# Optimization experiments

Hardware: AMD Instinct MI355X
Metric: run time of the kernel (lower is better)

The kernel has to match this reference:

```python
import jax, jax.numpy as jnp
import numpy as np

N_NODES = 50000
N_EDGES = 800000
IN_F, HID_F, OUT_F = 96, 96, 32


def setup_inputs() -> dict:
    key = jax.random.key(0)
    k1, k2, k3, k4, k5 = jax.random.split(key, 5)
    x = jax.random.normal(k1, (N_NODES, IN_F), dtype=jnp.float32)
    src = jax.random.randint(k2, (N_EDGES,), 0, N_NODES, dtype=jnp.int32)
    dst = jax.random.randint(k3, (N_EDGES,), 0, N_NODES, dtype=jnp.int32)
    W1 = jax.random.normal(k4, (IN_F, HID_F), dtype=jnp.float32) / np.sqrt(IN_F)
    b1 = jnp.zeros((HID_F,), dtype=jnp.float32)
    W2 = jax.random.normal(k5, (HID_F, OUT_F), dtype=jnp.float32) / np.sqrt(HID_F)
    b2 = jnp.zeros((OUT_F,), dtype=jnp.float32)
    return {"x": x, "src": src, "dst": dst, "W1": W1, "b1": b1, "W2": W2, "b2": b2}


def _graph_conv(src, dst, n_nodes, h, W, b):
    # DGL GraphConv, norm='both': D_out^{-1/2} A D_in^{-1/2} h W + b
    ones = jnp.ones((src.shape[0],), dtype=h.dtype)
    deg_out = jax.ops.segment_sum(ones, src, num_segments=n_nodes)  # src out-degree
    deg_in = jax.ops.segment_sum(ones, dst, num_segments=n_nodes)   # dst in-degree
    norm_src = jax.lax.rsqrt(jnp.maximum(deg_out, 1.0))
    norm_dst = jax.lax.rsqrt(jnp.maximum(deg_in, 1.0))
    h = h * norm_src[:, None]
    msg = h[src]                                                    # [E, F] gather
    agg = jax.ops.segment_sum(msg, dst, num_segments=n_nodes)       # [N, F] scatter-add
    agg = agg * norm_dst[:, None]
    return agg @ W + b


def reference(x, src, dst, W1, b1, W2, b2):
    n = x.shape[0]
    h = _graph_conv(src, dst, n, x, W1, b1)
    h = jax.nn.relu(h)
    h = _graph_conv(src, dst, n, h, W2, b2)
    return h
```

## Files before the change

### kernel.cpp

```cpp
#include <hip/hip_runtime.h>


constexpr int NN = 50000;
constexpr int NE = 800000;
constexpr int CAP = 64;
constexpr int NNP = 50048;
constexpr int NSL = 160;
constexpr int HWN = NNP / 8;
constexpr int HWB = NNP / 4;
constexpr int PREF_NB = (NN + 255) / 256;
constexpr int CVTW_NB = 48;
constexpr int FILL_NB = NSL;
constexpr int CVTX_NB = ((NN + 1) * 12 + 255) / 256;

using bf16x8 = __attribute__((ext_vector_type(8))) short;
using u16x8  = __attribute__((ext_vector_type(8))) unsigned short;
using f32x4  = __attribute__((ext_vector_type(4))) float;

__device__ __forceinline__ ushort f2b(float f) {
    unsigned u = __float_as_uint(f);
    u += 0x7FFFu + ((u >> 16) & 1u);
    return (ushort)(u >> 16);
}
__device__ __forceinline__ float b2f(ushort h) {
    return __uint_as_float(((unsigned)h) << 16);
}

__global__ void hist_kernel(const int* __restrict__ src, const int* __restrict__ dst,
                            unsigned char* __restrict__ pS, unsigned char* __restrict__ pD,
                            int ne) {
    __shared__ int binsS[HWN];
    __shared__ int binsD[HWN];
    const int sl = blockIdx.x;
    for (int i = threadIdx.x; i < HWN; i += 256) { binsS[i] = 0; binsD[i] = 0; }
    __syncthreads();
    const int per4 = (ne / NSL) / 4;
    const int i0 = sl * per4;
    const int4* src4 = (const int4*)src;
    const int4* dst4 = (const int4*)dst;
    for (int i = i0 + threadIdx.x; i < i0 + per4; i += 256) {
        int4 s = src4[i];
        int4 d = dst4[i];
        unsigned u;
        u = (unsigned)s.x; atomicAdd(binsS + (u >> 3), 1 << ((u & 7) * 4));
        u = (unsigned)s.y; atomicAdd(binsS + (u >> 3), 1 << ((u & 7) * 4));
        u = (unsigned)s.z; atomicAdd(binsS + (u >> 3), 1 << ((u & 7) * 4));
        u = (unsigned)s.w; atomicAdd(binsS + (u >> 3), 1 << ((u & 7) * 4));
        u = (unsigned)d.x; atomicAdd(binsD + (u >> 3), 1 << ((u & 7) * 4));
        u = (unsigned)d.y; atomicAdd(binsD + (u >> 3), 1 << ((u & 7) * 4));
        u = (unsigned)d.z; atomicAdd(binsD + (u >> 3), 1 << ((u & 7) * 4));
        u = (unsigned)d.w; atomicAdd(binsD + (u >> 3), 1 << ((u & 7) * 4));
    }
    __syncthreads();
    int* oS = (int*)(pS + (size_t)sl * NNP);
    int* oD = (int*)(pD + (size_t)sl * NNP);
    for (int t = threadIdx.x; t < HWN; t += 256) {
        int w = binsS[t];
        oS[2 * t]     = (w & 0xF) | ((w >> 4) & 0xF) << 8 | ((w >> 8) & 0xF) << 16 | ((w >> 12) & 0xF) << 24;
        oS[2 * t + 1] = ((w >> 16) & 0xF) | ((w >> 20) & 0xF) << 8 | ((w >> 24) & 0xF) << 16 | ((w >> 28) & 0xF) << 24;
        w = binsD[t];
        oD[2 * t]     = (w & 0xF) | ((w >> 4) & 0xF) << 8 | ((w >> 8) & 0xF) << 16 | ((w >> 12) & 0xF) << 24;
        oD[2 * t + 1] = ((w >> 16) & 0xF) | ((w >> 20) & 0xF) << 8 | ((w >> 24) & 0xF) << 16 | ((w >> 28) & 0xF) << 24;
    }
}

__global__ void prefix_cvtw_kernel(const unsigned char* __restrict__ pS,
                                   unsigned char* __restrict__ pD,
                                   float* __restrict__ ns, int* __restrict__ cnt,
                                   const float* __restrict__ W1, const float* __restrict__ W2,
                                   ushort* __restrict__ W1t, ushort* __restrict__ W2t, int n) {
    int b = blockIdx.x;
    if (b < PREF_NB) {
        int i = b * 256 + threadIdx.x;
        if (i >= n) return;
        int sS = 0, run = 0;
#pragma unroll 8
        for (int sl = 0; sl < NSL; ++sl) {
            sS += pS[(size_t)sl * NNP + i];
            int c = pD[(size_t)sl * NNP + i];
            pD[(size_t)sl * NNP + i] = (unsigned char)run;
            run += c;
        }
        ns[i] = rsqrtf(fmaxf((float)sS, 1.0f));
        cnt[i] = run;
    } else {
        int i = (b - PREF_NB) * 256 + threadIdx.x;
        if (i < 96 * 96) {
            int k = i / 96, c = i % 96;
            W1t[c * 96 + k] = f2b(W1[i]);
        } else {
            int j = i - 96 * 96;
            int k = j / 32, c = j % 32;
            W2t[c * 96 + k] = f2b(W2[j]);
        }
    }
}

__global__ void fill_cvtx_kernel(const int* __restrict__ src, const int* __restrict__ dst,
                                 const unsigned char* __restrict__ pD,
                                 ushort* __restrict__ slots,
                                 const float* __restrict__ x, const float* __restrict__ ns,
                                 ushort* __restrict__ xh, int ne, int n) {
    __shared__ int cur[HWB];
    int b = blockIdx.x;
    if (b < FILL_NB) {
        const int sl = b;
        const int* ip = (const int*)(pD + (size_t)sl * NNP);
        for (int t = threadIdx.x; t < HWB; t += 256) cur[t] = ip[t];
        __syncthreads();
        const int per4 = (ne / NSL) / 4;
        const int i0 = sl * per4;
        const int4* src4 = (const int4*)src;
        const int4* dst4 = (const int4*)dst;
        for (int i = i0 + threadIdx.x; i < i0 + per4; i += 256) {
            int4 d = dst4[i];
            int4 s = src4[i];
            unsigned u; int sh, old, p;
            u = (unsigned)d.x; sh = (u & 3) * 8; old = atomicAdd(cur + (u >> 2), 1 << sh);
            p = (old >> sh) & 0xFF; if (p < CAP) slots[((size_t)u << 6) + p] = (ushort)s.x;
            u = (unsigned)d.y; sh = (u & 3) * 8; old = atomicAdd(cur + (u >> 2), 1 << sh);
            p = (old >> sh) & 0xFF; if (p < CAP) slots[((size_t)u << 6) + p] = (ushort)s.y;
            u = (unsigned)d.z; sh = (u & 3) * 8; old = atomicAdd(cur + (u >> 2), 1 << sh);
            p = (old >> sh) & 0xFF; if (p < CAP) slots[((size_t)u << 6) + p] = (ushort)s.z;
            u = (unsigned)d.w; sh = (u & 3) * 8; old = atomicAdd(cur + (u >> 2), 1 << sh);
            p = (old >> sh) & 0xFF; if (p < CAP) slots[((size_t)u << 6) + p] = (ushort)s.w;
        }
    } else {
        int t = (b - FILL_NB) * 256 + threadIdx.x;
        if (t >= (n + 1) * 12) return;
        int r = t / 12;
        u16x8 o;
        if (r == n) {
#pragma unroll
            for (int u = 0; u < 8; ++u) o[u] = 0;
        } else {
            float s = ns[r];
            const float4* p = (const float4*)(x) + (size_t)t * 2;
            float4 v0 = p[0], v1 = p[1];
            o[0] = f2b(s * v0.x); o[1] = f2b(s * v0.y); o[2] = f2b(s * v0.z); o[3] = f2b(s * v0.w);
            o[4] = f2b(s * v1.x); o[5] = f2b(s * v1.y); o[6] = f2b(s * v1.z); o[7] = f2b(s * v1.w);
        }
        *(u16x8*)&xh[(size_t)t * 8] = o;
    }
}

__global__ void __launch_bounds__(256, 4) fused_aggemm(
        const ushort* __restrict__ xh, const int* __restrict__ cnt,
        const ushort* __restrict__ slots,
        const ushort* __restrict__ W1t, const ushort* __restrict__ W2t,
        const float* __restrict__ b1, const float* __restrict__ ns,
        ushort* __restrict__ t2h, int n) {
    __shared__ ushort Hl[64 * 104];
    const int rowbase0 = blockIdx.x * 64;

    for (int u = threadIdx.x; u < 768; u += 256) {
        int rl = u / 12, q = u % 12;
        int r = rowbase0 + rl;
        int deg = (r < n) ? min(cnt[r], CAP) : 0;
        const ushort* br = slots + ((size_t)r << 6);
        float acc[8] = {};
        for (int j0 = 0; j0 < deg; j0 += 8) {
            u16x8 sl8 = *(const u16x8*)(br + j0);
            int s0 = (j0 + 0 < deg) ? (int)sl8[0] : n;
            int s1 = (j0 + 1 < deg) ? (int)sl8[1] : n;
            int s2 = (j0 + 2 < deg) ? (int)sl8[2] : n;
            int s3 = (j0 + 3 < deg) ? (int)sl8[3] : n;
            int s4 = (j0 + 4 < deg) ? (int)sl8[4] : n;
            int s5 = (j0 + 5 < deg) ? (int)sl8[5] : n;
            int s6 = (j0 + 6 < deg) ? (int)sl8[6] : n;
            int s7 = (j0 + 7 < deg) ? (int)sl8[7] : n;
            u16x8 v0 = *(const u16x8*)&xh[(size_t)s0 * 96 + q * 8];
            u16x8 v1 = *(const u16x8*)&xh[(size_t)s1 * 96 + q * 8];
            u16x8 v2 = *(const u16x8*)&xh[(size_t)s2 * 96 + q * 8];
            u16x8 v3 = *(const u16x8*)&xh[(size_t)s3 * 96 + q * 8];
            u16x8 v4 = *(const u16x8*)&xh[(size_t)s4 * 96 + q * 8];
            u16x8 v5 = *(const u16x8*)&xh[(size_t)s5 * 96 + q * 8];
            u16x8 v6 = *(const u16x8*)&xh[(size_t)s6 * 96 + q * 8];
            u16x8 v7 = *(const u16x8*)&xh[(size_t)s7 * 96 + q * 8];
#pragma unroll
            for (int t = 0; t < 8; ++t) acc[t] += b2f(v0[t]);
#pragma unroll
            for (int t = 0; t < 8; ++t) acc[t] += b2f(v1[t]);
#pragma unroll
            for (int t = 0; t < 8; ++t) acc[t] += b2f(v2[t]);
#pragma unroll
            for (int t = 0; t < 8; ++t) acc[t] += b2f(v3[t]);
#pragma unroll
            for (int t = 0; t < 8; ++t) acc[t] += b2f(v4[t]);
#pragma unroll
            for (int t = 0; t < 8; ++t) acc[t] += b2f(v5[t]);
#pragma unroll
            for (int t = 0; t < 8; ++t) acc[t] += b2f(v6[t]);
#pragma unroll
            for (int t = 0; t < 8; ++t) acc[t] += b2f(v7[t]);
        }
        u16x8 o;
#pragma unroll
        for (int t = 0; t < 8; ++t) o[t] = f2b(acc[t]);
        *(u16x8*)&Hl[rl * 104 + q * 8] = o;
    }
    __syncthreads();

    const int lane = threadIdx.x & 63;
    const int w = threadIdx.x >> 6;
    const int rl = lane & 15, kg = lane >> 4;
    const ushort* hrow = &Hl[(w * 16 + rl) * 104 + kg * 8];

    bf16x8 a0 = *(const bf16x8*)(hrow);
    bf16x8 a1 = *(const bf16x8*)(hrow + 32);
    bf16x8 a2 = *(const bf16x8*)(hrow + 64);
    f32x4 acc1[6] = {};
#pragma unroll
    for (int nt = 0; nt < 6; ++nt) {
        const ushort* wr = W1t + (nt * 16 + rl) * 96 + kg * 8;
        acc1[nt] = __builtin_amdgcn_mfma_f32_16x16x32_bf16(a0, *(const bf16x8*)(wr),      acc1[nt], 0, 0, 0);
        acc1[nt] = __builtin_amdgcn_mfma_f32_16x16x32_bf16(a1, *(const bf16x8*)(wr + 32), acc1[nt], 0, 0, 0);
        acc1[nt] = __builtin_amdgcn_mfma_f32_16x16x32_bf16(a2, *(const bf16x8*)(wr + 64), acc1[nt], 0, 0, 0);
    }
    const int r0 = rowbase0 + w * 16 + kg * 4;
    float sj[4];
#pragma unroll
    for (int j = 0; j < 4; ++j) sj[j] = rsqrtf(fmaxf((float)cnt[r0 + j], 1.0f));
#pragma unroll
    for (int nt = 0; nt < 6; ++nt) {
        int col = nt * 16 + rl;
        float bc = b1[col];
#pragma unroll
        for (int j = 0; j < 4; ++j)
            Hl[(w * 16 + kg * 4 + j) * 104 + col] = f2b(fmaxf(acc1[nt][j] * sj[j] + bc, 0.f));
    }
    __syncthreads();

    bf16x8 h0 = *(const bf16x8*)(hrow);
    bf16x8 h1 = *(const bf16x8*)(hrow + 32);
    bf16x8 h2 = *(const bf16x8*)(hrow + 64);
    f32x4 acc2[2] = {};
#pragma unroll
    for (int nt = 0; nt < 2; ++nt) {
        const ushort* wr = W2t + (nt * 16 + rl) * 96 + kg * 8;
        acc2[nt] = __builtin_amdgcn_mfma_f32_16x16x32_bf16(h0, *(const bf16x8*)(wr),      acc2[nt], 0, 0, 0);
        acc2[nt] = __builtin_amdgcn_mfma_f32_16x16x32_bf16(h1, *(const bf16x8*)(wr + 32), acc2[nt], 0, 0, 0);
        acc2[nt] = __builtin_amdgcn_mfma_f32_16x16x32_bf16(h2, *(const bf16x8*)(wr + 64), acc2[nt], 0, 0, 0);
    }
    float sn[4];
#pragma unroll
    for (int j = 0; j < 4; ++j) sn[j] = ns[r0 + j];
#pragma unroll
    for (int nt = 0; nt < 2; ++nt) {
        int col = nt * 16 + rl;
#pragma unroll
        for (int j = 0; j < 4; ++j) {
            float val = (r0 + j < n) ? acc2[nt][j] * sn[j] : 0.f;
            t2h[(size_t)(r0 + j) * 32 + col] = f2b(val);
        }
    }
}

__global__ void agg2_kernel(const ushort* __restrict__ t2h, const float* __restrict__ b2,
                            const int* __restrict__ cnt, const ushort* __restrict__ slots,
                            float* __restrict__ out, int n) {
    int tid = blockIdx.x * 256 + threadIdx.x;
    int r = tid / 4, q = tid & 3;
    if (r >= n) return;
    int deg = min(cnt[r], CAP);
    const ushort* br = slots + ((size_t)r << 6);
    float acc[8] = {};
    for (int j0 = 0; j0 < deg; j0 += 8) {
        u16x8 sl8 = *(const u16x8*)(br + j0);
        int s0 = (j0 + 0 < deg) ? (int)sl8[0] : n;
        int s1 = (j0 + 1 < deg) ? (int)sl8[1] : n;
        int s2 = (j0 + 2 < deg) ? (int)sl8[2] : n;
        int s3 = (j0 + 3 < deg) ? (int)sl8[3] : n;
        int s4 = (j0 + 4 < deg) ? (int)sl8[4] : n;
        int s5 = (j0 + 5 < deg) ? (int)sl8[5] : n;
        int s6 = (j0 + 6 < deg) ? (int)sl8[6] : n;
        int s7 = (j0 + 7 < deg) ? (int)sl8[7] : n;
        u16x8 v0 = *(const u16x8*)&t2h[(size_t)s0 * 32 + q * 8];
        u16x8 v1 = *(const u16x8*)&t2h[(size_t)s1 * 32 + q * 8];
        u16x8 v2 = *(const u16x8*)&t2h[(size_t)s2 * 32 + q * 8];
        u16x8 v3 = *(const u16x8*)&t2h[(size_t)s3 * 32 + q * 8];
        u16x8 v4 = *(const u16x8*)&t2h[(size_t)s4 * 32 + q * 8];
        u16x8 v5 = *(const u16x8*)&t2h[(size_t)s5 * 32 + q * 8];
        u16x8 v6 = *(const u16x8*)&t2h[(size_t)s6 * 32 + q * 8];
        u16x8 v7 = *(const u16x8*)&t2h[(size_t)s7 * 32 + q * 8];
#pragma unroll
        for (int t = 0; t < 8; ++t) acc[t] += b2f(v0[t]);
#pragma unroll
        for (int t = 0; t < 8; ++t) acc[t] += b2f(v1[t]);
#pragma unroll
        for (int t = 0; t < 8; ++t) acc[t] += b2f(v2[t]);
#pragma unroll
        for (int t = 0; t < 8; ++t) acc[t] += b2f(v3[t]);
#pragma unroll
        for (int t = 0; t < 8; ++t) acc[t] += b2f(v4[t]);
#pragma unroll
        for (int t = 0; t < 8; ++t) acc[t] += b2f(v5[t]);
#pragma unroll
        for (int t = 0; t < 8; ++t) acc[t] += b2f(v6[t]);
#pragma unroll
        for (int t = 0; t < 8; ++t) acc[t] += b2f(v7[t]);
    }
    float sd = rsqrtf(fmaxf((float)deg, 1.0f));
    const float4* bb = (const float4*)(b2 + q * 8);
    float4 bv0 = bb[0], bv1 = bb[1];
    float4 o0, o1;
    o0.x = acc[0] * sd + bv0.x; o0.y = acc[1] * sd + bv0.y;
    o0.z = acc[2] * sd + bv0.z; o0.w = acc[3] * sd + bv0.w;
    o1.x = acc[4] * sd + bv1.x; o1.y = acc[5] * sd + bv1.y;
    o1.z = acc[6] * sd + bv1.z; o1.w = acc[7] * sd + bv1.w;
    float4* po = (float4*)&out[(size_t)r * 32 + q * 8];
    po[0] = o0; po[1] = o1;
}

extern "C" void kernel_launch(void* const* d_in, const int* in_sizes, int n_in,
                              void* d_out, int out_size, void* d_ws, size_t ws_size,
                              hipStream_t stream) {
    const float* x   = (const float*)d_in[0];
    const int*   src = (const int*)d_in[1];
    const int*   dst = (const int*)d_in[2];
    const float* W1  = (const float*)d_in[3];
    const float* b1  = (const float*)d_in[4];
    const float* W2  = (const float*)d_in[5];
    const float* b2  = (const float*)d_in[6];
    float* out = (float*)d_out;

    int*    cnt   = (int*)d_ws;
    float*  ns    = (float*)(cnt + NNP);
    ushort* slots = (ushort*)(ns + NNP);
    unsigned char* pS = (unsigned char*)(slots + (size_t)NN * CAP);
    unsigned char* pD = pS + (size_t)NSL * NNP;
    ushort* xh    = (ushort*)(pD + (size_t)NSL * NNP);
    ushort* t2h   = xh + (size_t)NNP * 96;
    ushort* W1t   = t2h + (size_t)NNP * 32;
    ushort* W2t   = W1t + 96 * 96;

    hist_kernel<<<NSL, 256, 0, stream>>>(src, dst, pS, pD, NE);
    prefix_cvtw_kernel<<<PREF_NB + CVTW_NB, 256, 0, stream>>>(pS, pD, ns, cnt, W1, W2, W1t, W2t, NN);
    fill_cvtx_kernel<<<FILL_NB + CVTX_NB, 256, 0, stream>>>(src, dst, pD, slots, x, ns, xh, NE, NN);

    fused_aggemm<<<NNP / 64, 256, 0, stream>>>(xh, cnt, slots, W1t, W2t, b1, ns, t2h, NN);
    agg2_kernel<<<(NN * 4 + 255) / 256, 256, 0, stream>>>(t2h, b2, cnt, slots, out, NN);
}
```

Baseline: 82.30 us.

## Split bf16 feature table into three 32-column planes and gather plane by plane

```diff
diff --git a/kernel.cpp b/kernel.cpp
--- a/kernel.cpp
+++ b/kernel.cpp
@@ -128,7 +128,8 @@
     } else {
         int t = (b - FILL_NB) * 256 + threadIdx.x;
         if (t >= (n + 1) * 12) return;
-        int r = t / 12;
+        int r = t / 12, q = t % 12;
+        int kb = q >> 2, qq = q & 3;
         u16x8 o;
         if (r == n) {
 #pragma unroll
@@ -140,7 +141,7 @@
             o[0] = f2b(s * v0.x); o[1] = f2b(s * v0.y); o[2] = f2b(s * v0.z); o[3] = f2b(s * v0.w);
             o[4] = f2b(s * v1.x); o[5] = f2b(s * v1.y); o[6] = f2b(s * v1.z); o[7] = f2b(s * v1.w);
         }
-        *(u16x8*)&xh[(size_t)t * 8] = o;
+        *(u16x8*)&xh[((size_t)kb * (NN + 64) + r) * 32 + qq * 8] = o;
     }
 }
 
@@ -153,53 +154,58 @@
     __shared__ ushort Hl[64 * 104];
     const int rowbase0 = blockIdx.x * 64;
 
-    for (int u = threadIdx.x; u < 768; u += 256) {
-        int rl = u / 12, q = u % 12;
-        int r = rowbase0 + rl;
+    const int grl = threadIdx.x >> 2;
+    const int gqq = threadIdx.x & 3;
+    {
+        int r = rowbase0 + grl;
         int deg = (r < n) ? min(cnt[r], CAP) : 0;
         const ushort* br = slots + ((size_t)r << 6);
-        float acc[8] = {};
-        for (int j0 = 0; j0 < deg; j0 += 8) {
-            u16x8 sl8 = *(const u16x8*)(br + j0);
-            int s0 = (j0 + 0 < deg) ? (int)sl8[0] : n;
-            int s1 = (j0 + 1 < deg) ? (int)sl8[1] : n;
-            int s2 = (j0 + 2 < deg) ? (int)sl8[2] : n;
-            int s3 = (j0 + 3 < deg) ? (int)sl8[3] : n;
-            int s4 = (j0 + 4 < deg) ? (int)sl8[4] : n;
-            int s5 = (j0 + 5 < deg) ? (int)sl8[5] : n;
-            int s6 = (j0 + 6 < deg) ? (int)sl8[6] : n;
-            int s7 = (j0 + 7 < deg) ? (int)sl8[7] : n;
-            u16x8 v0 = *(const u16x8*)&xh[(size_t)s0 * 96 + q * 8];
-            u16x8 v1 = *(const u16x8*)&xh[(size_t)s1 * 96 + q * 8];
-            u16x8 v2 = *(const u16x8*)&xh[(size_t)s2 * 96 + q * 8];
-            u16x8 v3 = *(const u16x8*)&xh[(size_t)s3 * 96 + q * 8];
-            u16x8 v4 = *(const u16x8*)&xh[(size_t)s4 * 96 + q * 8];
-            u16x8 v5 = *(const u16x8*)&xh[(size_t)s5 * 96 + q * 8];
-            u16x8 v6 = *(const u16x8*)&xh[(size_t)s6 * 96 + q * 8];
-            u16x8 v7 = *(const u16x8*)&xh[(size_t)s7 * 96 + q * 8];
-#pragma unroll
-            for (int t = 0; t < 8; ++t) acc[t] += b2f(v0[t]);
-#pragma unroll
-            for (int t = 0; t < 8; ++t) acc[t] += b2f(v1[t]);
-#pragma unroll
-            for (int t = 0; t < 8; ++t) acc[t] += b2f(v2[t]);
-#pragma unroll
-            for (int t = 0; t < 8; ++t) acc[t] += b2f(v3[t]);
-#pragma unroll
-            for (int t = 0; t < 8; ++t) acc[t] += b2f(v4[t]);
-#pragma unroll
-            for (int t = 0; t < 8; ++t) acc[t] += b2f(v5[t]);
-#pragma unroll
-            for (int t = 0; t < 8; ++t) acc[t] += b2f(v6[t]);
-#pragma unroll
-            for (int t = 0; t < 8; ++t) acc[t] += b2f(v7[t]);
-        }
-        u16x8 o;
-#pragma unroll
-        for (int t = 0; t < 8; ++t) o[t] = f2b(acc[t]);
-        *(u16x8*)&Hl[rl * 104 + q * 8] = o;
-    }
-    __syncthreads();
+#pragma unroll 1
+        for (int p = 0; p < 3; ++p) {
+            const ushort* xb = xh + (size_t)p * (NN + 64) * 32;
+            float acc[8] = {};
+            for (int j0 = 0; j0 < deg; j0 += 8) {
+                u16x8 sl8 = *(const u16x8*)(br + j0);
+                int s0 = (j0 + 0 < deg) ? (int)sl8[0] : n;
+                int s1 = (j0 + 1 < deg) ? (int)sl8[1] : n;
+                int s2 = (j0 + 2 < deg) ? (int)sl8[2] : n;
+                int s3 = (j0 + 3 < deg) ? (int)sl8[3] : n;
+                int s4 = (j0 + 4 < deg) ? (int)sl8[4] : n;
+                int s5 = (j0 + 5 < deg) ? (int)sl8[5] : n;
+                int s6 = (j0 + 6 < deg) ? (int)sl8[6] : n;
+                int s7 = (j0 + 7 < deg) ? (int)sl8[7] : n;
+                u16x8 v0 = *(const u16x8*)&xb[(size_t)s0 * 32 + gqq * 8];
+                u16x8 v1 = *(const u16x8*)&xb[(size_t)s1 * 32 + gqq * 8];
+                u16x8 v2 = *(const u16x8*)&xb[(size_t)s2 * 32 + gqq * 8];
+                u16x8 v3 = *(const u16x8*)&xb[(size_t)s3 * 32 + gqq * 8];
+                u16x8 v4 = *(const u16x8*)&xb[(size_t)s4 * 32 + gqq * 8];
+                u16x8 v5 = *(const u16x8*)&xb[(size_t)s5 * 32 + gqq * 8];
+                u16x8 v6 = *(const u16x8*)&xb[(size_t)s6 * 32 + gqq * 8];
+                u16x8 v7 = *(const u16x8*)&xb[(size_t)s7 * 32 + gqq * 8];
+#pragma unroll
+                for (int t = 0; t < 8; ++t) acc[t] += b2f(v0[t]);
+#pragma unroll
+                for (int t = 0; t < 8; ++t) acc[t] += b2f(v1[t]);
+#pragma unroll
+                for (int t = 0; t < 8; ++t) acc[t] += b2f(v2[t]);
+#pragma unroll
+                for (int t = 0; t < 8; ++t) acc[t] += b2f(v3[t]);
+#pragma unroll
+                for (int t = 0; t < 8; ++t) acc[t] += b2f(v4[t]);
+#pragma unroll
+                for (int t = 0; t < 8; ++t) acc[t] += b2f(v5[t]);
+#pragma unroll
+                for (int t = 0; t < 8; ++t) acc[t] += b2f(v6[t]);
+#pragma unroll
+                for (int t = 0; t < 8; ++t) acc[t] += b2f(v7[t]);
+            }
+            u16x8 o;
+#pragma unroll
+            for (int t = 0; t < 8; ++t) o[t] = f2b(acc[t]);
+            *(u16x8*)&Hl[grl * 104 + (p * 4 + gqq) * 8] = o;
+            __syncthreads();
+        }
+    }
 
     const int lane = threadIdx.x & 63;
     const int w = threadIdx.x >> 6;
@@ -330,7 +336,7 @@
     unsigned char* pS = (unsigned char*)(slots + (size_t)NN * CAP);
     unsigned char* pD = pS + (size_t)NSL * NNP;
     ushort* xh    = (ushort*)(pD + (size_t)NSL * NNP);
-    ushort* t2h   = xh + (size_t)NNP * 96;
+    ushort* t2h   = xh + (size_t)3 * (NN + 64) * 32;
     ushort* W1t   = t2h + (size_t)NNP * 32;
     ushort* W2t   = W1t + 96 * 96;
 
```

After: 84.25 us. 2.4% more time.
